# Performance work log

Hardware: AMD Instinct MI355X
Metric: run time of the kernel (lower is better)

Reference implementation:

```python
import jax, jax.numpy as jnp
import numpy as np

EPS = 1e-05
TEMP = 0.01
N_BINS = 15
N = 524288
C = 100


def setup_inputs() -> dict:
    key = jax.random.key(0)
    k1, k2 = jax.random.split(key)
    logits = jax.random.normal(k1, (N, C), dtype=jnp.float32)
    labels = jax.random.randint(k2, (N,), 0, C, dtype=jnp.int64)
    return {"logits": logits, "labels": labels}


def reference(logits, labels):
    # Faithful to torch: `predictions, confidences = torch.max(log_softmax, 1)`
    # -> predictions = max log-prob VALUES, confidences = argmax INDICES.
    logp = jax.nn.log_softmax(logits, axis=1)
    predictions = jnp.max(logp, axis=1)                      # [N] float
    confidences = jnp.argmax(logp, axis=1).astype(jnp.float32)  # [N] (indices as float)

    anchors = jnp.arange(1.0 / (2.0 * N_BINS), 1.0, 1.0 / N_BINS, dtype=jnp.float32)  # [B]

    # broadcasted -(c - a)^2 / temp, softmax over bins
    diff = -(confidences[:, None] - anchors[None, :]) ** 2 / TEMP  # [N, B]
    coeffs = jax.nn.softmax(diff, axis=1)                          # [N, B]

    sum_coeffs = jnp.sum(coeffs, axis=0)                           # [B]
    denom = jnp.maximum(sum_coeffs, EPS)

    bins_confidence = jnp.sum(confidences[:, None] * coeffs, axis=0) / denom

    accuracies = (predictions == labels.astype(predictions.dtype)).astype(jnp.float32)  # [N]
    bins_accuracy = jnp.sum(accuracies[:, None] * coeffs, axis=0) / denom

    # F.normalize(p=1): L1 normalization
    bin_weights = sum_coeffs / jnp.maximum(jnp.sum(jnp.abs(sum_coeffs)), EPS)

    ece = jnp.sqrt(jnp.dot((bins_confidence - bins_accuracy) ** 2, bin_weights))
    return ece
```

## Files before the change

kernel.cpp:

```cpp
#include <hip/hip_runtime.h>
#include <math.h>

#define NBINS 15
#define NCLS 100
#define ECE_EPS 1e-5f

__global__ __launch_bounds__(64) void ece_hist(const float* __restrict__ logits,
                                               const int* __restrict__ labels,
                                               int* __restrict__ g_cnt,
                                               float* __restrict__ g_acc,
                                               int n_rows) {
    __shared__ float s_rows[64 * NCLS];
    __shared__ int   s_cnt[NCLS];
    __shared__ float s_accs[NCLS];

    const int lane = threadIdx.x;
    #pragma unroll
    for (int i = lane; i < NCLS; i += 64) { s_cnt[i] = 0; s_accs[i] = 0.0f; }

    const int n_chunks = n_rows >> 6;
    for (int chunk = blockIdx.x; chunk < n_chunks; chunk += gridDim.x) {
        const float* gbase = logits + (size_t)chunk * (64 * NCLS);
        #pragma unroll
        for (int j = 0; j < 25; ++j) {
            __builtin_amdgcn_global_load_lds(
                (const __attribute__((address_space(1))) void*)(gbase + (size_t)(j * 64 + lane) * 4),
                (__attribute__((address_space(3))) void*)(&s_rows[j * 256]),
                16, 0, 0);
        }
        const int lab = labels[chunk * 64 + lane];
        __builtin_amdgcn_s_waitcnt(0);

        const float4* __restrict__ rp = (const float4*)&s_rows[lane * NCLS];
        float4 v[25];
        #pragma unroll
        for (int j = 0; j < 25; ++j) v[j] = rp[j];

        float m = -INFINITY; int mi = 0;
        #pragma unroll
        for (int j = 0; j < 25; ++j) {
            if (v[j].x > m) { m = v[j].x; mi = 4 * j;     }
            if (v[j].y > m) { m = v[j].y; mi = 4 * j + 1; }
            if (v[j].z > m) { m = v[j].z; mi = 4 * j + 2; }
            if (v[j].w > m) { m = v[j].w; mi = 4 * j + 3; }
        }
        float s0 = 0.0f, s1 = 0.0f, s2 = 0.0f, s3 = 0.0f;
        #pragma unroll
        for (int j = 0; j < 25; ++j) {
            s0 += __expf(v[j].x - m);
            s1 += __expf(v[j].y - m);
            s2 += __expf(v[j].z - m);
            s3 += __expf(v[j].w - m);
        }
        const float pred = -__logf((s0 + s1) + (s2 + s3));

        atomicAdd(&s_cnt[mi], 1);
        if (pred == (float)lab) atomicAdd(&s_accs[mi], 1.0f);
    }

    const int tail_start = n_chunks << 6;
    if (blockIdx.x == 0 && tail_start + lane < n_rows) {
        const float* row = logits + (size_t)(tail_start + lane) * NCLS;
        float m = -INFINITY; int mi = 0;
        for (int c = 0; c < NCLS; ++c) { const float x = row[c]; if (x > m) { m = x; mi = c; } }
        float s = 0.0f;
        for (int c = 0; c < NCLS; ++c) s += __expf(row[c] - m);
        const float pred = -__logf(s);
        atomicAdd(&s_cnt[mi], 1);
        if (pred == (float)labels[tail_start + lane]) atomicAdd(&s_accs[mi], 1.0f);
    }

    #pragma unroll
    for (int i = lane; i < NCLS; i += 64) {
        if (s_cnt[i])          atomicAdd(&g_cnt[i], s_cnt[i]);
        if (s_accs[i] != 0.0f) atomicAdd(&g_acc[i], s_accs[i]);
    }
}

__global__ void ece_final(const int* __restrict__ g_cnt,
                          const float* __restrict__ g_acc,
                          float* __restrict__ out) {
    __shared__ float s_bins[3 * NBINS];
    const int tid = threadIdx.x;
    if (tid < 3 * NBINS) s_bins[tid] = 0.0f;
    __syncthreads();

    if (tid < NCLS) {
        const float cnt  = (float)g_cnt[tid];
        const float accv = g_acc[tid];
        const float conf = (float)tid;
        float diff[NBINS];
        float dm = -INFINITY;
        #pragma unroll
        for (int b = 0; b < NBINS; ++b) {
            const float a = (float)(2 * b + 1) * (1.0f / 30.0f);
            const float d = conf - a;
            diff[b] = -(d * d) * 100.0f;
            dm = fmaxf(dm, diff[b]);
        }
        float es = 0.0f;
        float e[NBINS];
        #pragma unroll
        for (int b = 0; b < NBINS; ++b) { e[b] = __expf(diff[b] - dm); es += e[b]; }
        const float inv = 1.0f / es;
        #pragma unroll
        for (int b = 0; b < NBINS; ++b) {
            const float coeff = e[b] * inv;
            atomicAdd(&s_bins[b],             cnt * coeff);
            atomicAdd(&s_bins[NBINS + b],     conf * cnt * coeff);
            atomicAdd(&s_bins[2 * NBINS + b], accv * coeff);
        }
    }
    __syncthreads();

    if (tid == 0) {
        float total = 0.0f;
        #pragma unroll
        for (int b = 0; b < NBINS; ++b) total += fabsf(s_bins[b]);
        const float invw = 1.0f / fmaxf(total, ECE_EPS);
        float ece = 0.0f;
        #pragma unroll
        for (int b = 0; b < NBINS; ++b) {
            const float sc = s_bins[b];
            const float denom = fmaxf(sc, ECE_EPS);
            const float bc = s_bins[NBINS + b] / denom;
            const float ba = s_bins[2 * NBINS + b] / denom;
            const float d  = bc - ba;
            ece += d * d * (sc * invw);
        }
        out[0] = sqrtf(ece);
    }
}

extern "C" void kernel_launch(void* const* d_in, const int* in_sizes, int n_in,
                              void* d_out, int out_size, void* d_ws, size_t ws_size,
                              hipStream_t stream) {
    const float* logits = (const float*)d_in[0];
    const int*   labels = (const int*)d_in[1];
    int*   g_cnt = (int*)d_ws;
    float* g_acc = (float*)((char*)d_ws + NCLS * sizeof(int));
    float* outp  = (float*)d_out;
    const int n_rows = in_sizes[1];

    hipMemsetAsync(d_ws, 0, NCLS * (sizeof(int) + sizeof(float)), stream);
    ece_hist<<<2048, 64, 0, stream>>>(logits, labels, g_cnt, g_acc, n_rows);
    ece_final<<<1, 128, 0, stream>>>(g_cnt, g_acc, outp);
}
```

Before: 380.2 us.

## Double-buffer LDS row chunks with async prefetch and rotated reads

Adds a second LDS buffer so the next 64-row chunk is fetched with global_load_lds while the current chunk is processed, waiting only on the older batch of loads through a partial vmcnt. Each lane reads its row starting at a different float4 offset to reduce LDS bank conflicts, with a tie-break on the argmax so the first maximum is still chosen. The grid drops from 2048 to 768 blocks so each block runs more iterations and the prefetch has time to overlap. This doubles LDS per block and relies on hand-encoded waitcnt constants being correct.

```diff
diff --git a/kernel.cpp b/kernel.cpp
--- a/kernel.cpp
+++ b/kernel.cpp
@@ -5,12 +5,15 @@
 #define NCLS 100
 #define ECE_EPS 1e-5f
 
+#define WAIT_VM25 0x4F79
+#define WAIT_VM0  0x0F70
+
 __global__ __launch_bounds__(64) void ece_hist(const float* __restrict__ logits,
                                                const int* __restrict__ labels,
                                                int* __restrict__ g_cnt,
                                                float* __restrict__ g_acc,
                                                int n_rows) {
-    __shared__ float s_rows[64 * NCLS];
+    __shared__ float s_rows[2][64 * NCLS];
     __shared__ int   s_cnt[NCLS];
     __shared__ float s_accs[NCLS];
 
@@ -19,43 +22,69 @@
     for (int i = lane; i < NCLS; i += 64) { s_cnt[i] = 0; s_accs[i] = 0.0f; }
 
     const int n_chunks = n_rows >> 6;
-    for (int chunk = blockIdx.x; chunk < n_chunks; chunk += gridDim.x) {
+    const int rot = (lane >> 3) & 7;
+
+    int chunk = blockIdx.x;
+    if (chunk < n_chunks) {
         const float* gbase = logits + (size_t)chunk * (64 * NCLS);
         #pragma unroll
         for (int j = 0; j < 25; ++j) {
             __builtin_amdgcn_global_load_lds(
                 (const __attribute__((address_space(1))) void*)(gbase + (size_t)(j * 64 + lane) * 4),
-                (__attribute__((address_space(3))) void*)(&s_rows[j * 256]),
+                (__attribute__((address_space(3))) void*)(&s_rows[0][j * 256]),
                 16, 0, 0);
         }
+    }
+
+    int buf = 0;
+    while (chunk < n_chunks) {
+        const int next = chunk + gridDim.x;
         const int lab = labels[chunk * 64 + lane];
-        __builtin_amdgcn_s_waitcnt(0);
+        if (next < n_chunks) {
+            const float* gbase = logits + (size_t)next * (64 * NCLS);
+            #pragma unroll
+            for (int j = 0; j < 25; ++j) {
+                __builtin_amdgcn_global_load_lds(
+                    (const __attribute__((address_space(1))) void*)(gbase + (size_t)(j * 64 + lane) * 4),
+                    (__attribute__((address_space(3))) void*)(&s_rows[buf ^ 1][j * 256]),
+                    16, 0, 0);
+            }
+            __builtin_amdgcn_s_waitcnt(WAIT_VM25);
+        } else {
+            __builtin_amdgcn_s_waitcnt(WAIT_VM0);
+        }
 
-        const float4* __restrict__ rp = (const float4*)&s_rows[lane * NCLS];
-        float4 v[25];
-        #pragma unroll
-        for (int j = 0; j < 25; ++j) v[j] = rp[j];
+        const float4* __restrict__ rp = (const float4*)&s_rows[buf][lane * NCLS];
 
-        float m = -INFINITY; int mi = 0;
+        float m = -INFINITY; int mi = 1 << 30;
         #pragma unroll
         for (int j = 0; j < 25; ++j) {
-            if (v[j].x > m) { m = v[j].x; mi = 4 * j;     }
-            if (v[j].y > m) { m = v[j].y; mi = 4 * j + 1; }
-            if (v[j].z > m) { m = v[j].z; mi = 4 * j + 2; }
-            if (v[j].w > m) { m = v[j].w; mi = 4 * j + 3; }
+            int jj = j + rot; jj -= (jj >= 25) ? 25 : 0;
+            const float4 x = rp[jj];
+            const int base = 4 * jj;
+            if (x.x > m || (x.x == m && base     < mi)) { m = x.x; mi = base;     }
+            if (x.y > m || (x.y == m && base + 1 < mi)) { m = x.y; mi = base + 1; }
+            if (x.z > m || (x.z == m && base + 2 < mi)) { m = x.z; mi = base + 2; }
+            if (x.w > m || (x.w == m && base + 3 < mi)) { m = x.w; mi = base + 3; }
         }
+
         float s0 = 0.0f, s1 = 0.0f, s2 = 0.0f, s3 = 0.0f;
         #pragma unroll
         for (int j = 0; j < 25; ++j) {
-            s0 += __expf(v[j].x - m);
-            s1 += __expf(v[j].y - m);
-            s2 += __expf(v[j].z - m);
-            s3 += __expf(v[j].w - m);
+            int jj = j + rot; jj -= (jj >= 25) ? 25 : 0;
+            const float4 x = rp[jj];
+            s0 += __expf(x.x - m);
+            s1 += __expf(x.y - m);
+            s2 += __expf(x.z - m);
+            s3 += __expf(x.w - m);
         }
         const float pred = -__logf((s0 + s1) + (s2 + s3));
 
         atomicAdd(&s_cnt[mi], 1);
         if (pred == (float)lab) atomicAdd(&s_accs[mi], 1.0f);
+
+        buf ^= 1;
+        chunk = next;
     }
 
     const int tail_start = n_chunks << 6;
@@ -143,6 +172,6 @@
     const int n_rows = in_sizes[1];
 
     hipMemsetAsync(d_ws, 0, NCLS * (sizeof(int) + sizeof(float)), stream);
-    ece_hist<<<2048, 64, 0, stream>>>(logits, labels, g_cnt, g_acc, n_rows);
+    ece_hist<<<768, 64, 0, stream>>>(logits, labels, g_cnt, g_acc, n_rows);
     ece_final<<<1, 128, 0, stream>>>(g_cnt, g_acc, outp);
 }
```

Measured after the change: 389.7 us. 2.5% more time.

## Fuse final reduction into histogram kernel and rotate LDS reads to avoid bank conflicts

Applied to the files above, without the earlier changes.

The separate single-block finalize kernel is removed, and the last block to finish, found through an atomic done counter, computes the ECE from the global histogram. Each lane now starts its row's float4 reads from LDS at a different rotation to spread bank accesses, and it reads from LDS directly instead of holding the row in 25 float4 registers. The argmax tie-break is changed to pick the smallest index so the result does not depend on the rotated scan order. This saves one kernel launch and should reduce LDS bank conflicts and register pressure, at the cost of reading LDS twice and adding a fence and an atomic per block.

```diff
diff --git a/kernel.cpp b/kernel.cpp
--- a/kernel.cpp
+++ b/kernel.cpp
@@ -5,20 +5,26 @@
 #define NCLS 100
 #define ECE_EPS 1e-5f
 
+
 __global__ __launch_bounds__(64) void ece_hist(const float* __restrict__ logits,
                                                const int* __restrict__ labels,
                                                int* __restrict__ g_cnt,
                                                float* __restrict__ g_acc,
+                                               int* __restrict__ g_done,
+                                               float* __restrict__ out,
                                                int n_rows) {
     __shared__ float s_rows[64 * NCLS];
     __shared__ int   s_cnt[NCLS];
     __shared__ float s_accs[NCLS];
+    __shared__ float s_bins[3 * NBINS];
 
     const int lane = threadIdx.x;
     #pragma unroll
     for (int i = lane; i < NCLS; i += 64) { s_cnt[i] = 0; s_accs[i] = 0.0f; }
 
     const int n_chunks = n_rows >> 6;
+    const int rot = (lane >> 3) & 7;
+
     for (int chunk = blockIdx.x; chunk < n_chunks; chunk += gridDim.x) {
         const float* gbase = logits + (size_t)chunk * (64 * NCLS);
         #pragma unroll
@@ -32,25 +38,27 @@
         __builtin_amdgcn_s_waitcnt(0);
 
         const float4* __restrict__ rp = (const float4*)&s_rows[lane * NCLS];
-        float4 v[25];
-        #pragma unroll
-        for (int j = 0; j < 25; ++j) v[j] = rp[j];
 
-        float m = -INFINITY; int mi = 0;
+        float m = -INFINITY; int mi = 1 << 30;
         #pragma unroll
         for (int j = 0; j < 25; ++j) {
-            if (v[j].x > m) { m = v[j].x; mi = 4 * j;     }
-            if (v[j].y > m) { m = v[j].y; mi = 4 * j + 1; }
-            if (v[j].z > m) { m = v[j].z; mi = 4 * j + 2; }
-            if (v[j].w > m) { m = v[j].w; mi = 4 * j + 3; }
+            int jj = j + rot; jj -= (jj >= 25) ? 25 : 0;
+            const float4 x = rp[jj];
+            const int base = 4 * jj;
+            if (x.x > m || (x.x == m && base     < mi)) { m = x.x; mi = base;     }
+            if (x.y > m || (x.y == m && base + 1 < mi)) { m = x.y; mi = base + 1; }
+            if (x.z > m || (x.z == m && base + 2 < mi)) { m = x.z; mi = base + 2; }
+            if (x.w > m || (x.w == m && base + 3 < mi)) { m = x.w; mi = base + 3; }
         }
         float s0 = 0.0f, s1 = 0.0f, s2 = 0.0f, s3 = 0.0f;
         #pragma unroll
         for (int j = 0; j < 25; ++j) {
-            s0 += __expf(v[j].x - m);
-            s1 += __expf(v[j].y - m);
-            s2 += __expf(v[j].z - m);
-            s3 += __expf(v[j].w - m);
+            int jj = j + rot; jj -= (jj >= 25) ? 25 : 0;
+            const float4 x = rp[jj];
+            s0 += __expf(x.x - m);
+            s1 += __expf(x.y - m);
+            s2 += __expf(x.z - m);
+            s3 += __expf(x.w - m);
         }
         const float pred = -__logf((s0 + s1) + (s2 + s3));
 
@@ -65,9 +73,8 @@
         for (int c = 0; c < NCLS; ++c) { const float x = row[c]; if (x > m) { m = x; mi = c; } }
         float s = 0.0f;
         for (int c = 0; c < NCLS; ++c) s += __expf(row[c] - m);
-        const float pred = -__logf(s);
+        if (-__logf(s) == (float)labels[tail_start + lane]) atomicAdd(&s_accs[mi], 1.0f);
         atomicAdd(&s_cnt[mi], 1);
-        if (pred == (float)labels[tail_start + lane]) atomicAdd(&s_accs[mi], 1.0f);
     }
 
     #pragma unroll
@@ -75,20 +82,19 @@
         if (s_cnt[i])          atomicAdd(&g_cnt[i], s_cnt[i]);
         if (s_accs[i] != 0.0f) atomicAdd(&g_acc[i], s_accs[i]);
     }
-}
 
-__global__ void ece_final(const int* __restrict__ g_cnt,
-                          const float* __restrict__ g_acc,
-                          float* __restrict__ out) {
-    __shared__ float s_bins[3 * NBINS];
-    const int tid = threadIdx.x;
-    if (tid < 3 * NBINS) s_bins[tid] = 0.0f;
-    __syncthreads();
+    __threadfence();
+    int last = 0;
+    if (lane == 0) last = (atomicAdd(g_done, 1) == (int)gridDim.x - 1);
+    last = __shfl(last, 0);
+    if (!last) return;
+    __threadfence();
 
-    if (tid < NCLS) {
-        const float cnt  = (float)g_cnt[tid];
-        const float accv = g_acc[tid];
-        const float conf = (float)tid;
+    if (lane < 3 * NBINS) s_bins[lane] = 0.0f;
+    for (int c = lane; c < NCLS; c += 64) {
+        const float cnt  = (float)__hip_atomic_load(&g_cnt[c], __ATOMIC_ACQUIRE, __HIP_MEMORY_SCOPE_AGENT);
+        const float accv = __hip_atomic_load(&g_acc[c], __ATOMIC_ACQUIRE, __HIP_MEMORY_SCOPE_AGENT);
+        const float conf = (float)c;
         float diff[NBINS];
         float dm = -INFINITY;
         #pragma unroll
@@ -111,9 +117,7 @@
             atomicAdd(&s_bins[2 * NBINS + b], accv * coeff);
         }
     }
-    __syncthreads();
-
-    if (tid == 0) {
+    if (lane == 0) {
         float total = 0.0f;
         #pragma unroll
         for (int b = 0; b < NBINS; ++b) total += fabsf(s_bins[b]);
@@ -137,12 +141,12 @@
                               hipStream_t stream) {
     const float* logits = (const float*)d_in[0];
     const int*   labels = (const int*)d_in[1];
-    int*   g_cnt = (int*)d_ws;
-    float* g_acc = (float*)((char*)d_ws + NCLS * sizeof(int));
-    float* outp  = (float*)d_out;
+    int*   g_cnt  = (int*)d_ws;
+    float* g_acc  = (float*)((char*)d_ws + NCLS * sizeof(int));
+    int*   g_done = (int*)((char*)d_ws + NCLS * (sizeof(int) + sizeof(float)));
+    float* outp   = (float*)d_out;
     const int n_rows = in_sizes[1];
 
-    hipMemsetAsync(d_ws, 0, NCLS * (sizeof(int) + sizeof(float)), stream);
-    ece_hist<<<2048, 64, 0, stream>>>(logits, labels, g_cnt, g_acc, n_rows);
-    ece_final<<<1, 128, 0, stream>>>(g_cnt, g_acc, outp);
+    hipMemsetAsync(d_ws, 0, NCLS * (sizeof(int) + sizeof(float)) + sizeof(int), stream);
+    ece_hist<<<2048, 64, 0, stream>>>(logits, labels, g_cnt, g_acc, g_done, outp, n_rows);
 }
```

Measured after the change: 509.3 us. +34.0%, slower.
